# Performance work log

Measured on AMD Instinct MI355X. Metric: run time of the kernel, lower is better.

Reference implementation:

```python
import math
import jax, jax.numpy as jnp
import numpy as np
from jax.scipy.special import erfc

N = 768
L = 30.0
NTYPES = 10
EPS = 1e-8
COEF = 14.399645478425668  # 1e10 * e / (4*pi*epsilon_0) in eV*Angstrom
SQRT_2LOG = float(np.sqrt(-2.0 * np.log(1e-8)))  # from accuracy = 1e-8
SQRT2 = float(np.sqrt(2.0))


def _shift_grid(n):
    # all integer shifts in [-n, n]^3, shape ((2n+1)^3, 3)
    r = jnp.arange(-n, n + 1, dtype=jnp.float32)
    g = jnp.stack(jnp.meshgrid(r, r, r, indexing='ij'), axis=-1)
    return g.reshape(-1, 3)


def _ewald_energy_matrix(cell, pos, sigmas, nshift_real, nshift_recip):
    n = pos.shape[0]
    volume = jnp.abs(jnp.linalg.det(cell))
    eta = (volume ** 2 / n) ** (1.0 / 6.0) / jnp.sqrt(2.0 * jnp.pi)
    cutoff_real = SQRT_2LOG * eta
    cutoff_recip = SQRT_2LOG / eta

    # ---- real-space part ----
    disps = pos[None, :, :] - pos[:, None, :]                    # (n, n, 3)
    shifts = _shift_grid(nshift_real) @ cell                     # (S, 3)
    d = disps[None, :, :, :] + shifts[:, None, None, :]          # (S, n, n, 3)
    dist = jnp.linalg.norm(d, axis=-1)                           # (S, n, n)
    rmask = (dist > EPS) & (dist < cutoff_real)
    safe = jnp.where(rmask, dist, 1.0)
    gam = jnp.sqrt(sigmas[:, None] ** 2 + sigmas[None, :] ** 2)  # (n, n)
    val = (erfc(safe / (SQRT2 * eta)) - erfc(safe / (SQRT2 * gam[None]))) / safe
    e_real = COEF * jnp.sum(jnp.where(rmask, val, 0.0), axis=0)  # (n, n)

    # ---- reciprocal-space part (structure-factor form of sum_k w_k cos(k.(r_j-r_i))) ----
    recip = 2.0 * jnp.pi * jnp.linalg.inv(cell).T                # rows are reciprocal vectors
    ks = _shift_grid(nshift_recip) @ recip                       # (K, 3)
    klen = jnp.linalg.norm(ks, axis=-1)
    kmask = (klen > EPS) & (klen < cutoff_recip)
    safe_k = jnp.where(kmask, klen, 1.0)
    w = jnp.where(kmask, jnp.exp(-0.5 * (eta * safe_k) ** 2) / safe_k ** 2, 0.0)
    theta = ks @ pos.T                                           # (K, n)
    c, s = jnp.cos(theta), jnp.sin(theta)
    # cos(k.(r_j - r_i)) = c_ki c_kj + s_ki s_kj
    e_recip = COEF * (4.0 * jnp.pi / volume) * (c.T @ (w[:, None] * c) + s.T @ (w[:, None] * s))

    # ---- self part ----
    diag = -jnp.sqrt(2.0 / jnp.pi) / eta + 1.0 / (jnp.sqrt(jnp.pi) * sigmas)
    e_self = COEF * jnp.diag(diag)

    return e_real + e_recip + e_self


def setup_inputs() -> dict:
    key = jax.random.key(0)
    k1, k2, k3, k4 = jax.random.split(key, 4)
    pos = jax.random.uniform(k1, (N, 3), jnp.float32) * L
    cell = (L * jnp.eye(3, dtype=jnp.float32))[None]             # (1, 3, 3)
    charges = 0.3 * jax.random.normal(k2, (N, 1), jnp.float32)
    species_idx = jax.random.randint(k3, (N,), 0, NTYPES)
    sigma_table = 0.3 + 0.9 * jax.random.uniform(k4, (NTYPES,), jnp.float32)
    return {"pos": pos, "cell": cell, "charges": charges, "sigma_table": sigma_table,
            "species_idx": species_idx, "nshift_real": 1, "nshift_recip": 8}


def reference(pos, cell, charges, sigma_table, species_idx, nshift_real, nshift_recip):
    sigmas = sigma_table[species_idx]                            # (N,) gaussian widths per atom
    mat = _ewald_energy_matrix(cell[0], pos, sigmas, nshift_real, nshift_recip)
    q = charges[:, 0]
    e = 0.5 * jnp.sum(mat * q[:, None] * q[None, :])             # scale = 1.0
    return e.reshape(1, 1)
```

## Files before the change

### kernel.cpp

```cpp
#include <hip/hip_runtime.h>
#include <math.h>

#define COEF 14.399645478425668f
#define EPS2F 1e-16f
#define SQRT_2LOG 6.069708847f
#define INV_SQRT_2PI 0.3989422804014327f
#define TWO_PI 6.283185307179586f
#define INV_TWO_PI 0.15915494309189535f
#define SQRT_2_OVER_PI 0.7978845608028654f
#define INV_SQRT_PI 0.5641895835477563f

__device__ inline float erfc_fast(float x) {
    float t = 1.0f / fmaf(0.3275911f, x, 1.0f);
    float p = fmaf(t, 1.061405429f, -1.453152027f);
    p = fmaf(t, p, 1.421413741f);
    p = fmaf(t, p, -0.284496736f);
    p = fmaf(t, p, 0.254829592f);
    p *= t;
    return p * __expf(-x * x);
}

__device__ inline void cell_derived(const float* __restrict__ cell, int n,
                                    float& volume, float& eta, float M[3][3]) {
    float a00 = cell[0], a01 = cell[1], a02 = cell[2];
    float a10 = cell[3], a11 = cell[4], a12 = cell[5];
    float a20 = cell[6], a21 = cell[7], a22 = cell[8];
    float c00 = a11 * a22 - a12 * a21;
    float c01 = a12 * a20 - a10 * a22;
    float c02 = a10 * a21 - a11 * a20;
    float det = a00 * c00 + a01 * c01 + a02 * c02;
    volume = fabsf(det);
    eta = powf(volume * volume / (float)n, 1.0f / 6.0f) * INV_SQRT_2PI;
    float invdet = 1.0f / det;
    M[0][0] =  (a11 * a22 - a12 * a21) * invdet;
    M[0][1] = -(a01 * a22 - a02 * a21) * invdet;
    M[0][2] =  (a01 * a12 - a02 * a11) * invdet;
    M[1][0] = -(a10 * a22 - a12 * a20) * invdet;
    M[1][1] =  (a00 * a22 - a02 * a20) * invdet;
    M[1][2] = -(a00 * a12 - a02 * a10) * invdet;
    M[2][0] =  (a10 * a21 - a11 * a20) * invdet;
    M[2][1] = -(a00 * a21 - a01 * a20) * invdet;
    M[2][2] =  (a00 * a11 - a01 * a10) * invdet;
}

__global__ void zero_acc_kernel(double* acc) {
    if (threadIdx.x == 0 && blockIdx.x == 0) acc[0] = 0.0;
}

__global__ void ewald_fused_kernel(const float* __restrict__ pos,
                                   const float* __restrict__ cell,
                                   const float* __restrict__ charges,
                                   const float* __restrict__ sigma_table,
                                   const int* __restrict__ species,
                                   const int* __restrict__ p_nr,
                                   const int* __restrict__ p_nk,
                                   int n, int real_blocks,
                                   double* __restrict__ acc) {
    extern __shared__ float sm[];
    float* px = sm;
    float* py = sm + n;
    float* pz = sm + 2 * n;
    float* sq = sm + 3 * n;
    float* s2 = sm + 4 * n;
    float* red = sm + 5 * n;

    for (int t = threadIdx.x; t < n; t += blockDim.x) {
        px[t] = pos[3 * t + 0];
        py[t] = pos[3 * t + 1];
        pz[t] = pos[3 * t + 2];
        sq[t] = charges[t];
        float s = sigma_table[species[t]];
        s2[t] = s * s;
    }
    __syncthreads();

    float vol, eta, M[3][3];
    cell_derived(cell, n, vol, eta, M);

    int lane = threadIdx.x & 63;
    int wave = threadIdx.x >> 6;
    float thr_acc = 0.0f;
    double scale;

    if (blockIdx.x < real_blocks) {
        int nr = p_nr[0];
        float cutoff = SQRT_2LOG * eta;
        float cut2 = cutoff * cutoff;
        float inv_s2eta = 1.0f / (1.41421356237f * eta);
        float c00 = cell[0], c01 = cell[1], c02 = cell[2];
        float c10 = cell[3], c11 = cell[4], c12 = cell[5];
        float c20 = cell[6], c21 = cell[7], c22 = cell[8];

        long long T = (long long)n * (n + 1) / 2;
        long long p = (long long)blockIdx.x * blockDim.x + threadIdx.x;
        if (p < T) {
            float fp = 8.0f * (float)p + 1.0f;
            int i = (int)((sqrtf(fp) - 1.0f) * 0.5f);
            while ((long long)i * (i + 1) / 2 > p) --i;
            while ((long long)(i + 1) * (i + 2) / 2 <= p) ++i;
            int j = (int)(p - (long long)i * (i + 1) / 2);

            float dx = px[j] - px[i];
            float dy = py[j] - py[i];
            float dz = pz[j] - pz[i];
            float gam2 = s2[i] + s2[j];
            float inv_s2gam = rsqrtf(2.0f * gam2);
            float pacc = 0.0f;

            if (nr == 1) {
                #pragma unroll
                for (int a = -1; a <= 1; ++a) {
                    #pragma unroll
                    for (int b = -1; b <= 1; ++b) {
                        #pragma unroll
                        for (int c = -1; c <= 1; ++c) {
                            float ddx = dx + a * c00 + b * c10 + c * c20;
                            float ddy = dy + a * c01 + b * c11 + c * c21;
                            float ddz = dz + a * c02 + b * c12 + c * c22;
                            float r2 = fmaf(ddx, ddx, fmaf(ddy, ddy, ddz * ddz));
                            bool in = (r2 > EPS2F) & (r2 < cut2);
                            float r2s = in ? r2 : 1.0f;
                            float m = in ? 1.0f : 0.0f;
                            float rinv = rsqrtf(r2s);
                            float r = r2s * rinv;
                            float v = (erfc_fast(r * inv_s2eta) -
                                       erfc_fast(r * inv_s2gam)) * rinv;
                            pacc = fmaf(v, m, pacc);
                        }
                    }
                }
            } else {
                for (int a = -nr; a <= nr; ++a)
                for (int b = -nr; b <= nr; ++b)
                for (int c = -nr; c <= nr; ++c) {
                    float ddx = dx + a * c00 + b * c10 + c * c20;
                    float ddy = dy + a * c01 + b * c11 + c * c21;
                    float ddz = dz + a * c02 + b * c12 + c * c22;
                    float r2 = fmaf(ddx, ddx, fmaf(ddy, ddy, ddz * ddz));
                    bool in = (r2 > EPS2F) & (r2 < cut2);
                    float r2s = in ? r2 : 1.0f;
                    float m = in ? 1.0f : 0.0f;
                    float rinv = rsqrtf(r2s);
                    float r = r2s * rinv;
                    float v = (erfc_fast(r * inv_s2eta) -
                               erfc_fast(r * inv_s2gam)) * rinv;
                    pacc = fmaf(v, m, pacc);
                }
            }
            float w = (i == j) ? 1.0f : 2.0f;
            thr_acc = pacc * sq[i] * sq[j] * w;
        }
        scale = 0.5 * (double)COEF;
    } else {
        int nk = p_nk[0];
        int side = 2 * nk + 1;
        int K = side * side * side;
        float cutk = SQRT_2LOG / eta;
        float half_eta2 = 0.5f * eta * eta;

        int rb = blockIdx.x - real_blocks;
        int nrb = gridDim.x - real_blocks;
        int waves_per_block = blockDim.x >> 6;
        int gwave = rb * waves_per_block + wave;
        int nwaves = nrb * waves_per_block;

        for (int k = gwave; k < K; k += nwaves) {
            int a = k / (side * side) - nk;
            int rem = k % (side * side);
            int b = rem / side - nk;
            int c = rem % side - nk;
            float kx = TWO_PI * (M[0][0] * a + M[0][1] * b + M[0][2] * c);
            float ky = TWO_PI * (M[1][0] * a + M[1][1] * b + M[1][2] * c);
            float kz = TWO_PI * (M[2][0] * a + M[2][1] * b + M[2][2] * c);
            float k2 = fmaf(kx, kx, fmaf(ky, ky, kz * kz));
            float klen = sqrtf(k2);
            if (!(klen > 1e-8f && klen < cutk)) continue;
            float w = __expf(-half_eta2 * k2) / k2;
            float Sc = 0.0f, Ss = 0.0f;
            for (int i = lane; i < n; i += 64) {
                float th = fmaf(kx, px[i], fmaf(ky, py[i], kz * pz[i]));
                float sv, cv;
                __sincosf(th, &sv, &cv);
                float q = sq[i];
                Sc = fmaf(q, cv, Sc);
                Ss = fmaf(q, sv, Ss);
            }
            #pragma unroll
            for (int off = 32; off > 0; off >>= 1) {
                Sc += __shfl_down(Sc, off);
                Ss += __shfl_down(Ss, off);
            }
            if (lane == 0) thr_acc += w * (Sc * Sc + Ss * Ss);
        }
        scale = 0.5 * (double)COEF * (4.0 * 3.14159265358979323846 / (double)vol);
    }

    float v = thr_acc;
    #pragma unroll
    for (int off = 32; off > 0; off >>= 1) v += __shfl_down(v, off);
    if (lane == 0) red[wave] = v;
    __syncthreads();
    if (threadIdx.x == 0) {
        float tot = 0.0f;
        int nw = blockDim.x >> 6;
        for (int w = 0; w < nw; ++w) tot += red[w];
        if (tot != 0.0f) atomicAdd(acc, (double)tot * scale);
    }
}

__global__ void ewald_self_final_kernel(const float* __restrict__ cell,
                                        const float* __restrict__ charges,
                                        const float* __restrict__ sigma_table,
                                        const int* __restrict__ species,
                                        int n, const double* __restrict__ acc,
                                        float* __restrict__ out) {
    __shared__ float red[8];
    float vol, eta, M[3][3];
    cell_derived(cell, n, vol, eta, M);

    float ds = 0.0f;
    for (int i = threadIdx.x; i < n; i += blockDim.x) {
        float s = sigma_table[species[i]];
        float q = charges[i];
        float diag = -SQRT_2_OVER_PI / eta + INV_SQRT_PI / s;
        ds += 0.5f * COEF * q * q * diag;
    }
    float v = ds;
    #pragma unroll
    for (int off = 32; off > 0; off >>= 1) v += __shfl_down(v, off);
    int wave = threadIdx.x >> 6, lane = threadIdx.x & 63;
    if (lane == 0) red[wave] = v;
    __syncthreads();
    if (threadIdx.x == 0) {
        float tot = 0.0f;
        int nw = blockDim.x >> 6;
        for (int w = 0; w < nw; ++w) tot += red[w];
        out[0] = (float)(acc[0] + (double)tot);
    }
}

extern "C" void kernel_launch(void* const* d_in, const int* in_sizes, int n_in,
                              void* d_out, int out_size, void* d_ws, size_t ws_size,
                              hipStream_t stream) {
    const float* pos         = (const float*)d_in[0];
    const float* cell        = (const float*)d_in[1];
    const float* charges     = (const float*)d_in[2];
    const float* sigma_table = (const float*)d_in[3];
    const int*   species     = (const int*)d_in[4];
    const int*   p_nr        = (const int*)d_in[5];
    const int*   p_nk        = (const int*)d_in[6];
    int n = in_sizes[0] / 3;

    double* acc = (double*)d_ws;
    float* out = (float*)d_out;

    zero_acc_kernel<<<1, 64, 0, stream>>>(acc);

    long long T = (long long)n * (n + 1) / 2;
    int real_blocks = (int)((T + 255) / 256);
    int recip_blocks = 308;
    int total_blocks = real_blocks + recip_blocks;
    size_t sm_bytes = (size_t)(5 * n + 16) * sizeof(float);

    ewald_fused_kernel<<<total_blocks, 256, sm_bytes, stream>>>(
        pos, cell, charges, sigma_table, species, p_nr, p_nk,
        n, real_blocks, acc);

    ewald_self_final_kernel<<<1, 256, 0, stream>>>(
        cell, charges, sigma_table, species, n, acc, out);
}
```

Before: 93.93 us.

## Skip out-of-cutoff shifts per wave and replace atomics with per-block partials

The real-space shift loop now evaluates the erfc pair only when at least one lane in the wave has a shift inside the cutoff. The separate unrolled nr==1 path is dropped in favour of the generic loop. The double atomicAdd into one accumulator is replaced by per-block partial sums written to workspace, which the final kernel reduces in double. This removes the zero-init kernel launch. The wave-level branch adds divergence checks and loses full unrolling, which may cost some instruction-level parallelism.

```diff
diff --git a/kernel.cpp b/kernel.cpp
--- a/kernel.cpp
+++ b/kernel.cpp
@@ -6,7 +6,6 @@
 #define SQRT_2LOG 6.069708847f
 #define INV_SQRT_2PI 0.3989422804014327f
 #define TWO_PI 6.283185307179586f
-#define INV_TWO_PI 0.15915494309189535f
 #define SQRT_2_OVER_PI 0.7978845608028654f
 #define INV_SQRT_PI 0.5641895835477563f
 
@@ -43,10 +42,6 @@
     M[2][2] =  (a00 * a11 - a01 * a10) * invdet;
 }
 
-__global__ void zero_acc_kernel(double* acc) {
-    if (threadIdx.x == 0 && blockIdx.x == 0) acc[0] = 0.0;
-}
-
 __global__ void ewald_fused_kernel(const float* __restrict__ pos,
                                    const float* __restrict__ cell,
                                    const float* __restrict__ charges,
@@ -55,7 +50,7 @@
                                    const int* __restrict__ p_nr,
                                    const int* __restrict__ p_nk,
                                    int n, int real_blocks,
-                                   double* __restrict__ acc) {
+                                   double* __restrict__ partials) {
     extern __shared__ float sm[];
     float* px = sm;
     float* py = sm + n;
@@ -107,37 +102,15 @@
             float inv_s2gam = rsqrtf(2.0f * gam2);
             float pacc = 0.0f;
 
-            if (nr == 1) {
-                #pragma unroll
-                for (int a = -1; a <= 1; ++a) {
-                    #pragma unroll
-                    for (int b = -1; b <= 1; ++b) {
-                        #pragma unroll
-                        for (int c = -1; c <= 1; ++c) {
-                            float ddx = dx + a * c00 + b * c10 + c * c20;
-                            float ddy = dy + a * c01 + b * c11 + c * c21;
-                            float ddz = dz + a * c02 + b * c12 + c * c22;
-                            float r2 = fmaf(ddx, ddx, fmaf(ddy, ddy, ddz * ddz));
-                            bool in = (r2 > EPS2F) & (r2 < cut2);
-                            float r2s = in ? r2 : 1.0f;
-                            float m = in ? 1.0f : 0.0f;
-                            float rinv = rsqrtf(r2s);
-                            float r = r2s * rinv;
-                            float v = (erfc_fast(r * inv_s2eta) -
-                                       erfc_fast(r * inv_s2gam)) * rinv;
-                            pacc = fmaf(v, m, pacc);
-                        }
-                    }
-                }
-            } else {
-                for (int a = -nr; a <= nr; ++a)
-                for (int b = -nr; b <= nr; ++b)
-                for (int c = -nr; c <= nr; ++c) {
-                    float ddx = dx + a * c00 + b * c10 + c * c20;
-                    float ddy = dy + a * c01 + b * c11 + c * c21;
-                    float ddz = dz + a * c02 + b * c12 + c * c22;
-                    float r2 = fmaf(ddx, ddx, fmaf(ddy, ddy, ddz * ddz));
-                    bool in = (r2 > EPS2F) & (r2 < cut2);
+            for (int a = -nr; a <= nr; ++a)
+            for (int b = -nr; b <= nr; ++b)
+            for (int c = -nr; c <= nr; ++c) {
+                float ddx = dx + a * c00 + b * c10 + c * c20;
+                float ddy = dy + a * c01 + b * c11 + c * c21;
+                float ddz = dz + a * c02 + b * c12 + c * c22;
+                float r2 = fmaf(ddx, ddx, fmaf(ddy, ddy, ddz * ddz));
+                bool in = (r2 > EPS2F) & (r2 < cut2);
+                if (__any(in)) {
                     float r2s = in ? r2 : 1.0f;
                     float m = in ? 1.0f : 0.0f;
                     float rinv = rsqrtf(r2s);
@@ -204,38 +177,41 @@
         float tot = 0.0f;
         int nw = blockDim.x >> 6;
         for (int w = 0; w < nw; ++w) tot += red[w];
-        if (tot != 0.0f) atomicAdd(acc, (double)tot * scale);
-    }
-}
-
-__global__ void ewald_self_final_kernel(const float* __restrict__ cell,
-                                        const float* __restrict__ charges,
-                                        const float* __restrict__ sigma_table,
-                                        const int* __restrict__ species,
-                                        int n, const double* __restrict__ acc,
-                                        float* __restrict__ out) {
-    __shared__ float red[8];
+        partials[blockIdx.x] = (double)tot * scale;
+    }
+}
+
+__global__ void ewald_final_kernel(const float* __restrict__ cell,
+                                   const float* __restrict__ charges,
+                                   const float* __restrict__ sigma_table,
+                                   const int* __restrict__ species,
+                                   int n, int nparts,
+                                   const double* __restrict__ partials,
+                                   float* __restrict__ out) {
+    __shared__ double redd[8];
     float vol, eta, M[3][3];
     cell_derived(cell, n, vol, eta, M);
 
-    float ds = 0.0f;
+    double dsum = 0.0;
+    for (int i = threadIdx.x; i < nparts; i += blockDim.x)
+        dsum += partials[i];
     for (int i = threadIdx.x; i < n; i += blockDim.x) {
         float s = sigma_table[species[i]];
         float q = charges[i];
         float diag = -SQRT_2_OVER_PI / eta + INV_SQRT_PI / s;
-        ds += 0.5f * COEF * q * q * diag;
-    }
-    float v = ds;
+        dsum += (double)(0.5f * COEF * q * q * diag);
+    }
+    double v = dsum;
     #pragma unroll
     for (int off = 32; off > 0; off >>= 1) v += __shfl_down(v, off);
     int wave = threadIdx.x >> 6, lane = threadIdx.x & 63;
-    if (lane == 0) red[wave] = v;
+    if (lane == 0) redd[wave] = v;
     __syncthreads();
     if (threadIdx.x == 0) {
-        float tot = 0.0f;
+        double tot = 0.0;
         int nw = blockDim.x >> 6;
-        for (int w = 0; w < nw; ++w) tot += red[w];
-        out[0] = (float)(acc[0] + (double)tot);
+        for (int w = 0; w < nw; ++w) tot += redd[w];
+        out[0] = (float)tot;
     }
 }
 
@@ -251,10 +227,8 @@
     const int*   p_nk        = (const int*)d_in[6];
     int n = in_sizes[0] / 3;
 
-    double* acc = (double*)d_ws;
+    double* partials = (double*)d_ws;
     float* out = (float*)d_out;
-
-    zero_acc_kernel<<<1, 64, 0, stream>>>(acc);
 
     long long T = (long long)n * (n + 1) / 2;
     int real_blocks = (int)((T + 255) / 256);
@@ -264,8 +238,8 @@
 
     ewald_fused_kernel<<<total_blocks, 256, sm_bytes, stream>>>(
         pos, cell, charges, sigma_table, species, p_nr, p_nk,
-        n, real_blocks, acc);
-
-    ewald_self_final_kernel<<<1, 256, 0, stream>>>(
-        cell, charges, sigma_table, species, n, acc, out);
-}
+        n, real_blocks, partials);
+
+    ewald_final_kernel<<<1, 256, 0, stream>>>(
+        cell, charges, sigma_table, species, n, total_blocks, partials, out);
+}
```

New measurement: 85.78 us. -8.7%, faster.
